# Performance work log

Hardware: AMD Instinct MI355X
Metric: run time of the kernel (lower is better)

Reference implementation:

```python
import jax, jax.numpy as jnp
import numpy as np

B, H, L, E, MODES = 32, 8, 4096, 64, 64


def setup_inputs() -> dict:
    key = jax.random.key(0)
    kx, kw, ki = jax.random.split(key, 3)
    x = jax.random.normal(kx, (B, H, L, E), dtype=jnp.float32)
    # nn.Parameter(torch.randn(E, E, modes, 2) / sqrt(E))
    weights = jax.random.normal(kw, (E, E, MODES, 2), dtype=jnp.float32) / np.sqrt(E)
    # register_buffer: sorted random permutation of [0, seq_len//2) truncated to modes (unique)
    index = jnp.sort(jax.random.permutation(ki, L // 2)[:MODES]).astype(jnp.int64)
    return {"x": x, "weights": weights, "index": index}


def reference(x, weights, index):
    # x: [B, H, L, E]
    Bs, Hs, Ls, Es = x.shape
    xt = jnp.swapaxes(x, -1, -2)                 # [B, H, E, L]
    x_ft = jnp.fft.rfft(xt, axis=-1)             # [B, H, E, L//2+1] complex64
    w_c = weights[..., 0] + 1j * weights[..., 1]  # [E, E, modes] complex
    sel = x_ft[..., index]                       # gather selected modes: [B, H, E, modes]
    out_sel = jnp.einsum('bhei,eoi->bhoi', sel, w_c)  # [B, H, E_out, modes]
    out_ft = jnp.zeros_like(x_ft).at[..., index].set(out_sel)  # scatter into zero spectrum
    y = jnp.fft.irfft(out_ft, n=Ls, axis=-1)     # [B, H, E, L]
    return jnp.swapaxes(y, -1, -2)               # [B, H, L, E]
```

## Files before the change

kernel.cpp:

```cpp
#include <hip/hip_runtime.h>
#include <hip/hip_bf16.h>
#include <math.h>

#define LTOT   4096
#define EDIM   64
#define NMODES 64
#define BH     256
#define TWO_PI 6.28318530717958647692f

typedef float f32x4 __attribute__((ext_vector_type(4)));
typedef short s16x8 __attribute__((ext_vector_type(8)));

__device__ inline unsigned short f2bf(float f) {
    unsigned u = __builtin_bit_cast(unsigned, f);
    u += 0x7fff + ((u >> 16) & 1);
    return (unsigned short)(u >> 16);
}
__device__ inline unsigned packbf(float lo, float hi) {
    float2 t; t.x = lo; t.y = hi;
    __hip_bfloat162 h = __float22bfloat162_rn(t);
    unsigned r;
    __builtin_memcpy(&r, &h, 4);
    return r;
}

__global__ void k_tab_m(const int* __restrict__ index, unsigned short* __restrict__ Tm) {
    int k = blockIdx.x;
    int f = index[k];
    for (int l = threadIdx.x; l < LTOT; l += blockDim.x) {
        int m = (f * l) & (LTOT - 1);
        float th = (float)m * (TWO_PI / (float)LTOT);
        float s, c; sincosf(th, &s, &c);
        Tm[(size_t)(2 * k) * LTOT + l]     = f2bf(c);
        Tm[(size_t)(2 * k + 1) * LTOT + l] = f2bf(-s);
    }
}
__global__ void k_tab_t(const int* __restrict__ index, unsigned short* __restrict__ Tt) {
    int l = blockIdx.x * 4 + (threadIdx.x >> 6);
    int k = threadIdx.x & 63;
    int f = index[k];
    int m = (f * l) & (LTOT - 1);
    float th = (float)m * (TWO_PI / (float)LTOT);
    float s, c; sincosf(th, &s, &c);
    ((unsigned*)Tt)[l * 64 + k] = packbf(c, s);
}

#define S1P32 36
__global__ __launch_bounds__(256) void k_stage1(const float* __restrict__ x,
                                                const unsigned short* __restrict__ Tm,
                                                float* __restrict__ Xp) {
    int bh = blockIdx.x >> 2, part = blockIdx.x & 3;
    const float* xb = x + (size_t)bh * LTOT * EDIM;
    __shared__ unsigned xT[64 * S1P32];

    int t = threadIdx.x;
    int q = t & 15, lp = t >> 4;
    int lane = t & 63, wave = t >> 6;
    int r = lane & 15, kb8 = lane >> 4;
    int esb = (wave & 1) * 2;
    int mb  = (wave >> 1) * 64;

    f32x4 acc[2][4];
    #pragma unroll
    for (int i = 0; i < 2; ++i)
        #pragma unroll
        for (int n = 0; n < 4; ++n) acc[i][n] = (f32x4)0.f;

    for (int tile = 0; tile < 16; ++tile) {
        int l0 = part * 1024 + tile * 64;
        __syncthreads();
        const float* b0 = xb + (size_t)(l0 + 2 * lp) * EDIM + 4 * q;
        float4 a0 = *(const float4*)(b0);
        float4 a1 = *(const float4*)(b0 + EDIM);
        float4 a2 = *(const float4*)(b0 + 32 * EDIM);
        float4 a3 = *(const float4*)(b0 + 33 * EDIM);
        float A0[4] = {a0.x, a0.y, a0.z, a0.w};
        float A1[4] = {a1.x, a1.y, a1.z, a1.w};
        float A2[4] = {a2.x, a2.y, a2.z, a2.w};
        float A3[4] = {a3.x, a3.y, a3.z, a3.w};
        #pragma unroll
        for (int j = 0; j < 4; ++j) {
            int e = 4 * q + j;
            unsigned v = ((unsigned)(e >> 2) & 7u) << 2;
            xT[e * S1P32 + (( (unsigned)lp      ) ^ v)] = packbf(A0[j], A1[j]);
            xT[e * S1P32 + (( (unsigned)lp + 16u) ^ v)] = packbf(A2[j], A3[j]);
        }
        __syncthreads();
        #pragma unroll
        for (int kk = 0; kk < 2; ++kk) {
            s16x8 bf[4];
            #pragma unroll
            for (int ns = 0; ns < 4; ++ns) {
                int m = mb + ns * 16 + r;
                bf[ns] = *(const s16x8*)(Tm + (size_t)m * LTOT + (l0 + kk * 32 + kb8 * 8));
            }
            #pragma unroll
            for (int es = 0; es < 2; ++es) {
                int e = (esb + es) * 16 + r;
                unsigned v = ((unsigned)(e >> 2) & 7u) << 2;
                const unsigned* rowp = xT + e * S1P32;
                s16x8 af = *(const s16x8*)(rowp + (((unsigned)(kk * 16 + kb8 * 4)) ^ v));
                #pragma unroll
                for (int ns = 0; ns < 4; ++ns)
                    acc[es][ns] = __builtin_amdgcn_mfma_f32_16x16x32_bf16(af, bf[ns], acc[es][ns], 0, 0, 0);
            }
        }
    }
    float* Xb = Xp + ((size_t)part * BH + bh) * (64 * 128);
    #pragma unroll
    for (int es = 0; es < 2; ++es)
        #pragma unroll
        for (int ns = 0; ns < 4; ++ns)
            #pragma unroll
            for (int g = 0; g < 4; ++g) {
                int e = (esb + es) * 16 + kb8 * 4 + g;
                int m = mb + ns * 16 + r;
                Xb[e * 128 + m] = acc[es][ns][g];
            }
}

__global__ __launch_bounds__(512) void k_stage2(const float* __restrict__ Xp,
                                                const float2* __restrict__ w2,
                                                const int* __restrict__ index,
                                                unsigned* __restrict__ ABo) {
    int bh0 = blockIdx.x * 2;
    __shared__ float Xs[2][64 * 128];
    int t = threadIdx.x;

    #pragma unroll
    for (int bhi = 0; bhi < 2; ++bhi) {
        f32x4 a[4];
        #pragma unroll
        for (int i = 0; i < 4; ++i) a[i] = (f32x4)0.f;
        #pragma unroll
        for (int p = 0; p < 4; ++p) {
            const f32x4* src = (const f32x4*)(Xp + ((size_t)p * BH + bh0 + bhi) * 8192);
            #pragma unroll
            for (int i = 0; i < 4; ++i) a[i] += src[t + i * 512];
        }
        f32x4* dst = (f32x4*)Xs[bhi];
        #pragma unroll
        for (int i = 0; i < 4; ++i) dst[t + i * 512] = a[i];
    }
    __syncthreads();

    int k = t & 63, og = t >> 6;
    int f = index[k];
    float cc = (f == 0 ? 1.0f : 2.0f) / (float)LTOT;
    float aR[2][8] = {}, aI[2][8] = {};
    for (int e = 0; e < 64; ++e) {
        float2 X0 = *(const float2*)&Xs[0][e * 128 + 2 * k];
        float2 X1 = *(const float2*)&Xs[1][e * 128 + 2 * k];
        #pragma unroll
        for (int oi = 0; oi < 8; ++oi) {
            int o = og * 8 + oi;
            float2 wv = w2[((size_t)e * 64 + o) * 64 + k];
            aR[0][oi] += X0.x * wv.x - X0.y * wv.y;
            aI[0][oi] += X0.x * wv.y + X0.y * wv.x;
            aR[1][oi] += X1.x * wv.x - X1.y * wv.y;
            aI[1][oi] += X1.x * wv.y + X1.y * wv.x;
        }
    }
    #pragma unroll
    for (int bhi = 0; bhi < 2; ++bhi)
        #pragma unroll
        for (int oi = 0; oi < 8; ++oi) {
            int o = og * 8 + oi;
            float im = (f == 0) ? 0.0f : -cc * aI[bhi][oi];
            ABo[((size_t)(bh0 + bhi) * 64 + o) * 64 + k] = packbf(cc * aR[bhi][oi], im);
        }
}

#define S3P16 136
__global__ __launch_bounds__(256) void k_stage3(const unsigned short* __restrict__ Tt,
                                                const unsigned* __restrict__ ABo,
                                                float* __restrict__ y) {
    int bh = blockIdx.x >> 2, qtr = blockIdx.x & 3;
    __shared__ unsigned short ABl[64 * S3P16];
    int t = threadIdx.x;
    int lane = t & 63, wave = t >> 6;
    int r = lane & 15, kb8 = lane >> 4;

    {
        const unsigned* src = ABo + (size_t)bh * 4096;
        unsigned* dst = (unsigned*)ABl;
        #pragma unroll
        for (int i = 0; i < 16; ++i) {
            int idx = t + i * 256;
            int o = idx >> 6, c = idx & 63;
            dst[o * (S3P16 / 2) + c] = src[idx];
        }
    }
    __syncthreads();

    s16x8 afr[4][4];
    #pragma unroll
    for (int es = 0; es < 4; ++es)
        #pragma unroll
        for (int ks = 0; ks < 4; ++ks)
            afr[es][ks] = *(const s16x8*)(ABl + (es * 16 + r) * S3P16 + ks * 32 + kb8 * 8);

    for (int it = 0; it < 16; ++it) {
        int ltile = qtr * 1024 + it * 64 + wave * 16;
        s16x8 btf[4];
        #pragma unroll
        for (int ks = 0; ks < 4; ++ks)
            btf[ks] = *(const s16x8*)(Tt + (size_t)(ltile + r) * 128 + ks * 32 + kb8 * 8);
        f32x4 acc[4];
        #pragma unroll
        for (int es = 0; es < 4; ++es) acc[es] = (f32x4)0.f;
        #pragma unroll
        for (int ks = 0; ks < 4; ++ks)
            #pragma unroll
            for (int es = 0; es < 4; ++es)
                acc[es] = __builtin_amdgcn_mfma_f32_16x16x32_bf16(afr[es][ks], btf[ks], acc[es], 0, 0, 0);
        float* yb = y + ((size_t)bh * LTOT + ltile + r) * EDIM;
        #pragma unroll
        for (int es = 0; es < 4; ++es)
            *(f32x4*)(yb + es * 16 + kb8 * 4) = acc[es];
    }
}

extern "C" void kernel_launch(void* const* d_in, const int* in_sizes, int n_in,
                              void* d_out, int out_size, void* d_ws, size_t ws_size,
                              hipStream_t stream) {
    const float* x     = (const float*)d_in[0];
    const float* w     = (const float*)d_in[1];
    const int*   index = (const int*)d_in[2];
    float* y  = (float*)d_out;
    float* ws = (float*)d_ws;

    unsigned short* Tm = (unsigned short*)ws;
    unsigned short* Tt = (unsigned short*)(ws + 262144);
    float*          Xp = ws + 524288;
    unsigned*       ABo = (unsigned*)(ws + 8912896);

    hipLaunchKernelGGL(k_tab_m,  dim3(NMODES), dim3(256), 0, stream, index, Tm);
    hipLaunchKernelGGL(k_tab_t,  dim3(1024),   dim3(256), 0, stream, index, Tt);
    hipLaunchKernelGGL(k_stage1, dim3(BH * 4), dim3(256), 0, stream, x, Tm, Xp);
    hipLaunchKernelGGL(k_stage2, dim3(BH / 2), dim3(512), 0, stream, Xp, (const float2*)w, index, ABo);
    hipLaunchKernelGGL(k_stage3, dim3(BH * 4), dim3(256), 0, stream, Tt, ABo, y);
}
```

Baseline: 210.4 us.

## Fuse forward DFT, mode mixing, and inverse DFT into one kernel per bh

The three stage kernels become a single 1024-thread kernel with one block per (b,h). The forward projection accumulates over the full sequence in registers, with the next x tile prefetched into registers while the current one is multiplied. The partial spectra and mixed coefficients now stay in shared memory instead of going through global workspace. Weights are pre-packed to bf16 by a new table kernel, which halves weight traffic but adds rounding error. Only 256 blocks of 1024 threads are launched with launch_bounds(1024,1), so occupancy and parallelism drop, and the serialized 32-tile loop may limit throughput.

```diff
diff --git a/kernel.cpp b/kernel.cpp
--- a/kernel.cpp
+++ b/kernel.cpp
@@ -23,6 +23,9 @@
     __builtin_memcpy(&r, &h, 4);
     return r;
 }
+__device__ inline float bf2f(unsigned lo16) {
+    return __builtin_bit_cast(float, lo16 << 16);
+}
 
 __global__ void k_tab_m(const int* __restrict__ index, unsigned short* __restrict__ Tm) {
     int k = blockIdx.x;
@@ -44,180 +47,131 @@
     float s, c; sincosf(th, &s, &c);
     ((unsigned*)Tt)[l * 64 + k] = packbf(c, s);
 }
+__global__ void k_wtab(const float* __restrict__ w, unsigned* __restrict__ wt) {
+    int i = blockIdx.x * 256 + threadIdx.x;
+    float2 v = ((const float2*)w)[i];
+    wt[i] = packbf(v.x, v.y);
+}
 
-#define S1P32 36
-__global__ __launch_bounds__(256) void k_stage1(const float* __restrict__ x,
-                                                const unsigned short* __restrict__ Tm,
-                                                float* __restrict__ Xp) {
-    int bh = blockIdx.x >> 2, part = blockIdx.x & 3;
+__global__ __launch_bounds__(1024, 1) void k_fused(const float* __restrict__ x,
+                                                   const unsigned short* __restrict__ Tm,
+                                                   const unsigned short* __restrict__ Tt,
+                                                   const unsigned* __restrict__ wtab,
+                                                   const int* __restrict__ index,
+                                                   float* __restrict__ y) {
+    int bh = blockIdx.x;
     const float* xb = x + (size_t)bh * LTOT * EDIM;
-    __shared__ unsigned xT[64 * S1P32];
+
+    __shared__ unsigned xT[64 * 68];
+    __shared__ float    Xs[64 * 132];
+    __shared__ unsigned ABl[64 * 68];
 
     int t = threadIdx.x;
-    int q = t & 15, lp = t >> 4;
-    int lane = t & 63, wave = t >> 6;
+    int lane = t & 63, w = t >> 6;
     int r = lane & 15, kb8 = lane >> 4;
-    int esb = (wave & 1) * 2;
-    int mb  = (wave >> 1) * 64;
+    int es = w & 3, ms = w >> 2;
 
-    f32x4 acc[2][4];
-    #pragma unroll
-    for (int i = 0; i < 2; ++i)
-        #pragma unroll
-        for (int n = 0; n < 4; ++n) acc[i][n] = (f32x4)0.f;
+    int lp = t >> 4;
+    int q  = t & 15;
+    unsigned swzW = ((unsigned)(q & 7)) << 2;
+    unsigned swzR = (((unsigned)(es & 1)) << 4) + (((unsigned)(r >> 2)) << 2);
 
-    for (int tile = 0; tile < 16; ++tile) {
-        int l0 = part * 1024 + tile * 64;
-        __syncthreads();
-        const float* b0 = xb + (size_t)(l0 + 2 * lp) * EDIM + 4 * q;
-        float4 a0 = *(const float4*)(b0);
-        float4 a1 = *(const float4*)(b0 + EDIM);
-        float4 a2 = *(const float4*)(b0 + 32 * EDIM);
-        float4 a3 = *(const float4*)(b0 + 33 * EDIM);
-        float A0[4] = {a0.x, a0.y, a0.z, a0.w};
-        float A1[4] = {a1.x, a1.y, a1.z, a1.w};
-        float A2[4] = {a2.x, a2.y, a2.z, a2.w};
-        float A3[4] = {a3.x, a3.y, a3.z, a3.w};
-        #pragma unroll
-        for (int j = 0; j < 4; ++j) {
-            int e = 4 * q + j;
-            unsigned v = ((unsigned)(e >> 2) & 7u) << 2;
-            xT[e * S1P32 + (( (unsigned)lp      ) ^ v)] = packbf(A0[j], A1[j]);
-            xT[e * S1P32 + (( (unsigned)lp + 16u) ^ v)] = packbf(A2[j], A3[j]);
+    f32x4 acc[2]; acc[0] = (f32x4)0.f; acc[1] = (f32x4)0.f;
+
+    float4 a0, a1;
+    {
+        const float* b0 = xb + (size_t)(2 * lp) * EDIM + 4 * q;
+        a0 = *(const float4*)b0;
+        a1 = *(const float4*)(b0 + EDIM);
+    }
+    for (int tile = 0; tile < 32; ++tile) {
+        int l0 = tile * 128;
+        {
+            float A0[4] = {a0.x, a0.y, a0.z, a0.w};
+            float A1[4] = {a1.x, a1.y, a1.z, a1.w};
+            #pragma unroll
+            for (int j = 0; j < 4; ++j) {
+                int e = 4 * q + j;
+                xT[e * 68 + ((unsigned)lp ^ swzW)] = packbf(A0[j], A1[j]);
+            }
         }
         __syncthreads();
+        if (tile + 1 < 32) {
+            const float* b0 = xb + (size_t)(l0 + 128 + 2 * lp) * EDIM + 4 * q;
+            a0 = *(const float4*)b0;
+            a1 = *(const float4*)(b0 + EDIM);
+        }
         #pragma unroll
-        for (int kk = 0; kk < 2; ++kk) {
-            s16x8 bf[4];
+        for (int kk = 0; kk < 4; ++kk) {
+            s16x8 af = *(const s16x8*)(xT + (es * 16 + r) * 68 +
+                                       (((unsigned)(kk * 16 + kb8 * 4)) ^ swzR));
             #pragma unroll
-            for (int ns = 0; ns < 4; ++ns) {
-                int m = mb + ns * 16 + r;
-                bf[ns] = *(const s16x8*)(Tm + (size_t)m * LTOT + (l0 + kk * 32 + kb8 * 8));
-            }
-            #pragma unroll
-            for (int es = 0; es < 2; ++es) {
-                int e = (esb + es) * 16 + r;
-                unsigned v = ((unsigned)(e >> 2) & 7u) << 2;
-                const unsigned* rowp = xT + e * S1P32;
-                s16x8 af = *(const s16x8*)(rowp + (((unsigned)(kk * 16 + kb8 * 4)) ^ v));
-                #pragma unroll
-                for (int ns = 0; ns < 4; ++ns)
-                    acc[es][ns] = __builtin_amdgcn_mfma_f32_16x16x32_bf16(af, bf[ns], acc[es][ns], 0, 0, 0);
+            for (int ns = 0; ns < 2; ++ns) {
+                int m = ms * 32 + ns * 16 + r;
+                s16x8 bf = *(const s16x8*)(Tm + (size_t)m * LTOT + l0 + kk * 32 + kb8 * 8);
+                acc[ns] = __builtin_amdgcn_mfma_f32_16x16x32_bf16(af, bf, acc[ns], 0, 0, 0);
             }
         }
+        __syncthreads();
     }
-    float* Xb = Xp + ((size_t)part * BH + bh) * (64 * 128);
     #pragma unroll
-    for (int es = 0; es < 2; ++es)
+    for (int ns = 0; ns < 2; ++ns)
         #pragma unroll
-        for (int ns = 0; ns < 4; ++ns)
-            #pragma unroll
-            for (int g = 0; g < 4; ++g) {
-                int e = (esb + es) * 16 + kb8 * 4 + g;
-                int m = mb + ns * 16 + r;
-                Xb[e * 128 + m] = acc[es][ns][g];
-            }
-}
-
-__global__ __launch_bounds__(512) void k_stage2(const float* __restrict__ Xp,
-                                                const float2* __restrict__ w2,
-                                                const int* __restrict__ index,
-                                                unsigned* __restrict__ ABo) {
-    int bh0 = blockIdx.x * 2;
-    __shared__ float Xs[2][64 * 128];
-    int t = threadIdx.x;
-
-    #pragma unroll
-    for (int bhi = 0; bhi < 2; ++bhi) {
-        f32x4 a[4];
-        #pragma unroll
-        for (int i = 0; i < 4; ++i) a[i] = (f32x4)0.f;
-        #pragma unroll
-        for (int p = 0; p < 4; ++p) {
-            const f32x4* src = (const f32x4*)(Xp + ((size_t)p * BH + bh0 + bhi) * 8192);
-            #pragma unroll
-            for (int i = 0; i < 4; ++i) a[i] += src[t + i * 512];
-        }
-        f32x4* dst = (f32x4*)Xs[bhi];
-        #pragma unroll
-        for (int i = 0; i < 4; ++i) dst[t + i * 512] = a[i];
-    }
+        for (int g = 0; g < 4; ++g)
+            Xs[(es * 16 + kb8 * 4 + g) * 132 + ms * 32 + ns * 16 + r] = acc[ns][g];
     __syncthreads();
 
-    int k = t & 63, og = t >> 6;
-    int f = index[k];
-    float cc = (f == 0 ? 1.0f : 2.0f) / (float)LTOT;
-    float aR[2][8] = {}, aI[2][8] = {};
-    for (int e = 0; e < 64; ++e) {
-        float2 X0 = *(const float2*)&Xs[0][e * 128 + 2 * k];
-        float2 X1 = *(const float2*)&Xs[1][e * 128 + 2 * k];
+    {
+        int k = lane;
+        int og = w;
+        int f = index[k];
+        float cc = (f == 0 ? 1.0f : 2.0f) / (float)LTOT;
+        float aR[4] = {}, aI[4] = {};
+        for (int e = 0; e < 64; ++e) {
+            float2 X = *(const float2*)&Xs[e * 132 + 2 * k];
+            #pragma unroll
+            for (int oi = 0; oi < 4; ++oi) {
+                unsigned wv = wtab[((size_t)(e * 64 + og * 4 + oi)) * 64 + k];
+                float wr = bf2f(wv & 0xffffu);
+                float wi = bf2f(wv >> 16);
+                aR[oi] += X.x * wr - X.y * wi;
+                aI[oi] += X.x * wi + X.y * wr;
+            }
+        }
         #pragma unroll
-        for (int oi = 0; oi < 8; ++oi) {
-            int o = og * 8 + oi;
-            float2 wv = w2[((size_t)e * 64 + o) * 64 + k];
-            aR[0][oi] += X0.x * wv.x - X0.y * wv.y;
-            aI[0][oi] += X0.x * wv.y + X0.y * wv.x;
-            aR[1][oi] += X1.x * wv.x - X1.y * wv.y;
-            aI[1][oi] += X1.x * wv.y + X1.y * wv.x;
-        }
-    }
-    #pragma unroll
-    for (int bhi = 0; bhi < 2; ++bhi)
-        #pragma unroll
-        for (int oi = 0; oi < 8; ++oi) {
-            int o = og * 8 + oi;
-            float im = (f == 0) ? 0.0f : -cc * aI[bhi][oi];
-            ABo[((size_t)(bh0 + bhi) * 64 + o) * 64 + k] = packbf(cc * aR[bhi][oi], im);
-        }
-}
-
-#define S3P16 136
-__global__ __launch_bounds__(256) void k_stage3(const unsigned short* __restrict__ Tt,
-                                                const unsigned* __restrict__ ABo,
-                                                float* __restrict__ y) {
-    int bh = blockIdx.x >> 2, qtr = blockIdx.x & 3;
-    __shared__ unsigned short ABl[64 * S3P16];
-    int t = threadIdx.x;
-    int lane = t & 63, wave = t >> 6;
-    int r = lane & 15, kb8 = lane >> 4;
-
-    {
-        const unsigned* src = ABo + (size_t)bh * 4096;
-        unsigned* dst = (unsigned*)ABl;
-        #pragma unroll
-        for (int i = 0; i < 16; ++i) {
-            int idx = t + i * 256;
-            int o = idx >> 6, c = idx & 63;
-            dst[o * (S3P16 / 2) + c] = src[idx];
+        for (int oi = 0; oi < 4; ++oi) {
+            int o = og * 4 + oi;
+            float im = (f == 0) ? 0.0f : -cc * aI[oi];
+            ABl[o * 68 + k] = packbf(cc * aR[oi], im);
         }
     }
     __syncthreads();
 
     s16x8 afr[4][4];
     #pragma unroll
-    for (int es = 0; es < 4; ++es)
+    for (int es2 = 0; es2 < 4; ++es2)
         #pragma unroll
         for (int ks = 0; ks < 4; ++ks)
-            afr[es][ks] = *(const s16x8*)(ABl + (es * 16 + r) * S3P16 + ks * 32 + kb8 * 8);
+            afr[es2][ks] = *(const s16x8*)(ABl + (es2 * 16 + r) * 68 + ks * 16 + kb8 * 4);
 
     for (int it = 0; it < 16; ++it) {
-        int ltile = qtr * 1024 + it * 64 + wave * 16;
+        int ltile = w * 256 + it * 16;
         s16x8 btf[4];
         #pragma unroll
         for (int ks = 0; ks < 4; ++ks)
             btf[ks] = *(const s16x8*)(Tt + (size_t)(ltile + r) * 128 + ks * 32 + kb8 * 8);
-        f32x4 acc[4];
+        f32x4 oa[4];
         #pragma unroll
-        for (int es = 0; es < 4; ++es) acc[es] = (f32x4)0.f;
+        for (int es2 = 0; es2 < 4; ++es2) oa[es2] = (f32x4)0.f;
         #pragma unroll
         for (int ks = 0; ks < 4; ++ks)
             #pragma unroll
-            for (int es = 0; es < 4; ++es)
-                acc[es] = __builtin_amdgcn_mfma_f32_16x16x32_bf16(afr[es][ks], btf[ks], acc[es], 0, 0, 0);
+            for (int es2 = 0; es2 < 4; ++es2)
+                oa[es2] = __builtin_amdgcn_mfma_f32_16x16x32_bf16(afr[es2][ks], btf[ks], oa[es2], 0, 0, 0);
         float* yb = y + ((size_t)bh * LTOT + ltile + r) * EDIM;
         #pragma unroll
-        for (int es = 0; es < 4; ++es)
-            *(f32x4*)(yb + es * 16 + kb8 * 4) = acc[es];
+        for (int es2 = 0; es2 < 4; ++es2)
+            *(f32x4*)(yb + es2 * 16 + kb8 * 4) = oa[es2];
     }
 }
 
@@ -225,19 +179,17 @@
                               void* d_out, int out_size, void* d_ws, size_t ws_size,
                               hipStream_t stream) {
     const float* x     = (const float*)d_in[0];
-    const float* w     = (const float*)d_in[1];
+    const float* wgt   = (const float*)d_in[1];
     const int*   index = (const int*)d_in[2];
     float* y  = (float*)d_out;
     float* ws = (float*)d_ws;
 
     unsigned short* Tm = (unsigned short*)ws;
     unsigned short* Tt = (unsigned short*)(ws + 262144);
-    float*          Xp = ws + 524288;
-    unsigned*       ABo = (unsigned*)(ws + 8912896);
+    unsigned*       wt = (unsigned*)(ws + 524288);
 
-    hipLaunchKernelGGL(k_tab_m,  dim3(NMODES), dim3(256), 0, stream, index, Tm);
-    hipLaunchKernelGGL(k_tab_t,  dim3(1024),   dim3(256), 0, stream, index, Tt);
-    hipLaunchKernelGGL(k_stage1, dim3(BH * 4), dim3(256), 0, stream, x, Tm, Xp);
-    hipLaunchKernelGGL(k_stage2, dim3(BH / 2), dim3(512), 0, stream, Xp, (const float2*)w, index, ABo);
-    hipLaunchKernelGGL(k_stage3, dim3(BH * 4), dim3(256), 0, stream, Tt, ABo, y);
+    hipLaunchKernelGGL(k_tab_m, dim3(NMODES), dim3(256), 0, stream, index, Tm);
+    hipLaunchKernelGGL(k_tab_t, dim3(1024),   dim3(256), 0, stream, index, Tt);
+    hipLaunchKernelGGL(k_wtab,  dim3(1024),   dim3(256), 0, stream, wgt, wt);
+    hipLaunchKernelGGL(k_fused, dim3(BH),     dim3(1024), 0, stream, x, Tm, Tt, wt, index, y);
 }
```

Measured after the change: 238.5 us. +13.4%, slower.
